# Optimization experiments

Measured on AMD Instinct MI355X. Metric: run time of the kernel, lower is better.

The kernel has to match this reference:

```python
import jax, jax.numpy as jnp
import numpy as np

B, N, F_IN = 2, 2048, 256
HEADS, F_OUT = 8, 32
NEG_SLOPE = 0.01  # torch F.leaky_relu default


def setup_inputs() -> dict:
    key = jax.random.key(0)
    k1, k2, k3, k4 = jax.random.split(key, 4)
    stdv = 1.0 / np.sqrt(F_OUT * HEADS)
    h = jax.random.normal(k1, (B, N, F_IN), dtype=jnp.float32)
    adj = jax.random.uniform(k2, (B, N, N), dtype=jnp.float32)
    W = jax.random.normal(k3, (F_IN, F_OUT * HEADS), dtype=jnp.float32) * stdv
    a = jax.random.normal(k4, (2 * F_OUT, 1), dtype=jnp.float32) * stdv
    return {"h": h, "adj": adj, "W": W, "a": a}


def reference(h, adj, W, a):
    # adj is accepted by the original forward but never used (dense attention).
    b, n, _ = h.shape
    f = a.shape[0] // 2
    heads = W.shape[1] // f
    Wh = (h @ W).reshape(b, n, heads, f)            # [b,n,h,f]
    a1 = a[:f, 0]                                    # attends to source i
    a2 = a[f:, 0]                                    # attends to target j
    e1 = jnp.einsum('bnhf,f->bhn', Wh, a1)           # [b,h,n]
    e2 = jnp.einsum('bnhf,f->bhn', Wh, a2)           # [b,h,n]
    # e[b,h,i,j] = leaky_relu(a1.Wh_i + a2.Wh_j) == a^T [Wh_i || Wh_j]
    e = jax.nn.leaky_relu(e1[:, :, :, None] + e2[:, :, None, :], NEG_SLOPE)
    att = jax.nn.softmax(e, axis=-1)                 # softmax over neighbors j
    h_prime = jnp.einsum('bhij,bjhf->bihf', att, Wh)  # [b,n,h,f]
    return h_prime.reshape(b, n, heads * f)
```

## Files before the change

kernel.cpp:

```cpp
#include <hip/hip_runtime.h>
#include <math.h>

#define BATCH 2
#define NTOK  2048
#define FIN   256
#define HEADS 8
#define FOUT  32
#define BH    (BATCH*HEADS)
#define NCOL  (HEADS*FOUT)
#define ROWS  (BATCH*NTOK)

typedef _Float16 f16;
typedef _Float16 f16x8 __attribute__((ext_vector_type(8)));
typedef float    f32x4 __attribute__((ext_vector_type(4)));

static const size_t OFF_E1   = 1048576;
static const size_t OFF_E2   = OFF_E1 + 32768;
static const size_t OFF_SKEY = OFF_E2 + 32768;
static const size_t OFF_SIDX = OFF_SKEY + 32768;
static const size_t OFF_W1S  = OFF_SIDX + 32768;
static const size_t OFF_W2S  = OFF_W1S + 32768;
static const size_t OFF_S1   = OFF_W2S + 32768;
static const size_t OFF_P2   = OFF_S1 + 32784;
static const size_t OFF_V1   = OFF_P2 + 32784;
static const size_t OFF_P2V  = OFF_V1 + 16u*2049u*32u;
static const size_t OFF_PART = OFF_V1;

__global__ __launch_bounds__(512) void k_mm(const float* __restrict__ h,
                                            const float* __restrict__ W,
                                            const float* __restrict__ av,
                                            float* __restrict__ Wh,
                                            float* __restrict__ e1, float* __restrict__ e2) {
    const int tid  = threadIdx.x;
    const int hh   = tid >> 6;
    const int lane = tid & 63;
    const int r    = lane & 15;
    const int q    = lane >> 4;
    const int row0 = blockIdx.x * 16;
    const int colA = hh * 32;

    const float* pa = h + (size_t)(row0 + r) * FIN + q * 8;
    const float HS = 16.0f, WS = 4096.0f;

    f32x4 acc[2];
    acc[0] = (f32x4){0.f,0.f,0.f,0.f};
    acc[1] = (f32x4){0.f,0.f,0.f,0.f};

    for (int ks = 0; ks < 8; ++ks) {
        const int kb = ks * 32;
        const float4 a0 = *(const float4*)(pa + kb);
        const float4 a1 = *(const float4*)(pa + kb + 4);
        const float ax[8] = {a0.x,a0.y,a0.z,a0.w,a1.x,a1.y,a1.z,a1.w};
        f16x8 ahi, alo;
        #pragma unroll
        for (int j = 0; j < 8; ++j) {
            float xv = ax[j] * HS;
            f16 hv = (f16)xv;
            ahi[j] = hv; alo[j] = (f16)(xv - (float)hv);
        }
        f16x8 bhi[2], blo[2];
        #pragma unroll
        for (int t = 0; t < 2; ++t) {
            const float* pb = W + (size_t)(kb + q * 8) * NCOL + colA + t * 16 + r;
            #pragma unroll
            for (int j = 0; j < 8; ++j) {
                float xv = pb[(size_t)j * NCOL] * WS;
                f16 hv = (f16)xv;
                bhi[t][j] = hv; blo[t][j] = (f16)(xv - (float)hv);
            }
        }
        #pragma unroll
        for (int t = 0; t < 2; ++t) {
            acc[t] = __builtin_amdgcn_mfma_f32_16x16x32_f16(ahi, bhi[t], acc[t], 0, 0, 0);
            acc[t] = __builtin_amdgcn_mfma_f32_16x16x32_f16(ahi, blo[t], acc[t], 0, 0, 0);
            acc[t] = __builtin_amdgcn_mfma_f32_16x16x32_f16(alo, bhi[t], acc[t], 0, 0, 0);
        }
    }

    const float SC = 1.0f / 65536.0f;
    acc[0] *= SC; acc[1] *= SC;

    #pragma unroll
    for (int t = 0; t < 2; ++t)
        #pragma unroll
        for (int g = 0; g < 4; ++g)
            Wh[(size_t)(row0 + q * 4 + g) * NCOL + colA + t * 16 + r] = acc[t][g];

    const float a10 = av[r], a11 = av[16 + r];
    const float a20 = av[32 + r], a21 = av[48 + r];
    float p1[4], p2[4];
    #pragma unroll
    for (int g = 0; g < 4; ++g) {
        p1[g] = acc[0][g] * a10 + acc[1][g] * a11;
        p2[g] = acc[0][g] * a20 + acc[1][g] * a21;
    }
    #pragma unroll
    for (int m = 1; m < 16; m <<= 1)
        #pragma unroll
        for (int g = 0; g < 4; ++g) {
            p1[g] += __shfl_xor(p1[g], m, 64);
            p2[g] += __shfl_xor(p2[g], m, 64);
        }
    if (r == 0) {
        #pragma unroll
        for (int g = 0; g < 4; ++g) {
            const int row = row0 + q * 4 + g;
            const int b   = row >> 11;
            const int n   = row & (NTOK - 1);
            e1[(b * HEADS + hh) * NTOK + n] = p1[g];
            e2[(b * HEADS + hh) * NTOK + n] = p2[g];
        }
    }
}

__device__ __forceinline__ unsigned long long sortkey(float f, int j) {
    unsigned int b = __float_as_uint(f);
    unsigned int u = (b & 0x80000000u) ? ~b : (b | 0x80000000u);
    return ((unsigned long long)u << 32) | (unsigned int)(NTOK - 1 - j);
}

__global__ __launch_bounds__(256) void k_rank8(const float* __restrict__ e2g,
                                               int* __restrict__ partial) {
    __shared__ alignas(16) unsigned long long ch[256];
    const int tid = threadIdx.x;
    const int bh  = blockIdx.x;
    const int kt  = blockIdx.y;
    const int jh  = blockIdx.z;
    const int kbase = kt * 256;
    ch[tid] = sortkey(e2g[bh * NTOK + kbase + tid], kbase + tid);
    __syncthreads();

    const int j0 = jh * 1024 + tid * 4;
    const float4 mv = *(const float4*)(e2g + bh * NTOK + j0);
    const unsigned long long my0 = sortkey(mv.x, j0);
    const unsigned long long my1 = sortkey(mv.y, j0 + 1);
    const unsigned long long my2 = sortkey(mv.z, j0 + 2);
    const unsigned long long my3 = sortkey(mv.w, j0 + 3);
    int r0 = 0, r1 = 0, r2 = 0, r3 = 0;
    const ulonglong2* c2 = (const ulonglong2*)ch;
    #pragma unroll 8
    for (int qq = 0; qq < 128; ++qq) {
        ulonglong2 v = c2[qq];
        r0 += (v.x > my0) + (v.y > my0);
        r1 += (v.x > my1) + (v.y > my1);
        r2 += (v.x > my2) + (v.y > my2);
        r3 += (v.x > my3) + (v.y > my3);
    }
    *(int4*)(partial + (size_t)(kt * BH + bh) * NTOK + j0) = make_int4(r0, r1, r2, r3);
}

__global__ __launch_bounds__(256) void k_scatter(const float* __restrict__ e2g,
                                                 const int* __restrict__ partial,
                                                 float* __restrict__ skey,
                                                 int* __restrict__ sidx,
                                                 float* __restrict__ w1s,
                                                 float* __restrict__ w2s) {
    const int tid = threadIdx.x;
    const int bh  = blockIdx.x;
    const int jt  = blockIdx.y;
    const int j   = jt * 256 + tid;
    int rank = 0;
    #pragma unroll
    for (int kt = 0; kt < 8; ++kt)
        rank += partial[(size_t)(kt * BH + bh) * NTOK + j];
    const float my = e2g[bh * NTOK + j];
    skey[bh * NTOK + rank] = my;
    sidx[bh * NTOK + rank] = j;
    w1s[bh * NTOK + rank]  = expf(my);
    w2s[bh * NTOK + rank]  = expf(0.01f * my);
}

__global__ __launch_bounds__(1024) void k_vscan(const float* __restrict__ Wh,
                                                const int* __restrict__ sidx,
                                                const float* __restrict__ w1s,
                                                const float* __restrict__ w2s,
                                                float* __restrict__ V1,
                                                float* __restrict__ P2V,
                                                float* __restrict__ S1,
                                                float* __restrict__ P2) {
    __shared__ float4 wtot[16];
    __shared__ float4 woff[16];
    const int t    = threadIdx.x;
    const int lane = t & 63;
    const int wv   = t >> 6;
    const int fg   = blockIdx.x;
    const int bh   = blockIdx.y;
    const int b    = bh >> 3;
    const int hh   = bh & 7;
    const int j0   = 2 * t;

    const float w1_0 = w1s[bh * NTOK + j0], w1_1 = w1s[bh * NTOK + j0 + 1];
    const float w2_0 = w2s[bh * NTOK + j0], w2_1 = w2s[bh * NTOK + j0 + 1];
    float4 g0, g1;
    if (fg < 8) {
        const int sj0 = sidx[bh * NTOK + j0];
        const int sj1 = sidx[bh * NTOK + j0 + 1];
        g0 = *(const float4*)(Wh + (size_t)(b * NTOK + sj0) * NCOL + hh * FOUT + fg * 4);
        g1 = *(const float4*)(Wh + (size_t)(b * NTOK + sj1) * NCOL + hh * FOUT + fg * 4);
    } else {
        g0 = make_float4(1.f, 0.f, 0.f, 0.f);
        g1 = make_float4(1.f, 0.f, 0.f, 0.f);
    }

    #pragma unroll 1
    for (int z = 0; z < 2; ++z) {
        const float w0  = z ? w2_0 : w1_0;
        const float w1v = z ? w2_1 : w1_1;
        float4 v0 = make_float4(w0 * g0.x,  w0 * g0.y,  w0 * g0.z,  w0 * g0.w);
        float4 v1 = make_float4(w1v * g1.x, w1v * g1.y, w1v * g1.z, w1v * g1.w);

        float4 s = make_float4(v0.x + v1.x, v0.y + v1.y, v0.z + v1.z, v0.w + v1.w);
        #pragma unroll
        for (int d = 1; d < 64; d <<= 1) {
            float ux = __shfl_up(s.x, (unsigned)d, 64);
            float uy = __shfl_up(s.y, (unsigned)d, 64);
            float uz = __shfl_up(s.z, (unsigned)d, 64);
            float uw = __shfl_up(s.w, (unsigned)d, 64);
            if (lane >= d) { s.x += ux; s.y += uy; s.z += uz; s.w += uw; }
        }
        float4 pair = make_float4(v0.x + v1.x, v0.y + v1.y, v0.z + v1.z, v0.w + v1.w);
        float4 excl = make_float4(s.x - pair.x, s.y - pair.y, s.z - pair.z, s.w - pair.w);
        if (lane == 63) wtot[wv] = s;
        __syncthreads();
        if (t < 16) {
            float4 ws = wtot[t];
            float4 inc = ws;
            #pragma unroll
            for (int d = 1; d < 16; d <<= 1) {
                float ux = __shfl_up(inc.x, (unsigned)d, 16);
                float uy = __shfl_up(inc.y, (unsigned)d, 16);
                float uz = __shfl_up(inc.z, (unsigned)d, 16);
                float uw = __shfl_up(inc.w, (unsigned)d, 16);
                if ((t & 15) >= d) { inc.x += ux; inc.y += uy; inc.z += uz; inc.w += uw; }
            }
            woff[t] = make_float4(inc.x - ws.x, inc.y - ws.y, inc.z - ws.z, inc.w - ws.w);
        }
        __syncthreads();

        float4 base = woff[wv];
        float4 i0 = make_float4(base.x + excl.x + v0.x, base.y + excl.y + v0.y,
                                base.z + excl.z + v0.z, base.w + excl.w + v0.w);
        float4 i1 = make_float4(i0.x + v1.x, i0.y + v1.y, i0.z + v1.z, i0.w + v1.w);

        if (fg < 8) {
            float* dst = z ? P2V : V1;
            float* plane = dst + ((size_t)bh * 8 + fg) * (2049u * 4u);
            *(float4*)(plane + (size_t)(j0 + 1) * 4) = i0;
            *(float4*)(plane + (size_t)(j0 + 2) * 4) = i1;
            if (t == 0)
                *(float4*)plane = make_float4(0.f, 0.f, 0.f, 0.f);
        } else {
            float* dst = z ? P2 : S1;
            dst[bh * 2049 + j0 + 1] = i0.x;
            dst[bh * 2049 + j0 + 2] = i1.x;
            if (t == 0) dst[bh * 2049] = 0.f;
        }
        __syncthreads();
    }
}

__global__ __launch_bounds__(256) void k_out(const float* __restrict__ skey,
                                             const float* __restrict__ e1g,
                                             const float* __restrict__ S1,
                                             const float* __restrict__ P2,
                                             const float* __restrict__ V1,
                                             const float* __restrict__ P2V,
                                             float* __restrict__ out) {
    __shared__ float keys[NTOK];
    const int tid = threadIdx.x;
    const int it  = blockIdx.x;
    const int bh  = blockIdx.y;
    const int b   = bh >> 3;
    const int hh  = bh & 7;
    #pragma unroll
    for (int q = 0; q < 8; ++q)
        keys[q * 256 + tid] = skey[bh * NTOK + q * 256 + tid];
    __syncthreads();

    const int i  = it * 32 + (tid >> 3);
    const int fg = tid & 7;
    const float e1v = e1g[bh * NTOK + i];
    const float th  = -e1v;
    int lo = 0, hi = NTOK;
    while (lo < hi) {
        int mid = (lo + hi) >> 1;
        if (keys[mid] > th) lo = mid + 1; else hi = mid;
    }
    const int k = lo;
    const float A = expf(e1v);
    const float C = expf(0.01f * e1v);
    const float s1  = S1[bh * 2049 + k];
    const float p2k = P2[bh * 2049 + k];
    const float p2t = P2[bh * 2049 + 2048];
    const float l   = A * s1 + C * (p2t - p2k);
    const float inv = 1.0f / l;
    const float* v1p  = V1  + ((size_t)bh * 8 + fg) * (2049u * 4u);
    const float* p2vp = P2V + ((size_t)bh * 8 + fg) * (2049u * 4u);
    float4 v1   = *(const float4*)(v1p  + (size_t)k * 4);
    float4 p2v  = *(const float4*)(p2vp + (size_t)k * 4);
    float4 p2vt = *(const float4*)(p2vp + (size_t)2048 * 4);
    float4 o;
    o.x = (A * v1.x + C * (p2vt.x - p2v.x)) * inv;
    o.y = (A * v1.y + C * (p2vt.y - p2v.y)) * inv;
    o.z = (A * v1.z + C * (p2vt.z - p2v.z)) * inv;
    o.w = (A * v1.w + C * (p2vt.w - p2v.w)) * inv;
    *(float4*)(out + (size_t)(b * NTOK + i) * NCOL + hh * FOUT + fg * 4) = o;
}

extern "C" void kernel_launch(void* const* d_in, const int* in_sizes, int n_in,
                              void* d_out, int out_size, void* d_ws, size_t ws_size,
                              hipStream_t stream) {
    const float* h = (const float*)d_in[0];
    const float* W = (const float*)d_in[2];
    const float* a = (const float*)d_in[3];
    float* out = (float*)d_out;
    float* ws  = (float*)d_ws;

    float* Wh   = ws;
    float* e1   = ws + OFF_E1;
    float* e2   = ws + OFF_E2;
    float* skey = ws + OFF_SKEY;
    int*   sidx = (int*)(ws + OFF_SIDX);
    float* w1s  = ws + OFF_W1S;
    float* w2s  = ws + OFF_W2S;
    float* S1   = ws + OFF_S1;
    float* P2   = ws + OFF_P2;
    float* V1   = ws + OFF_V1;
    float* P2V  = ws + OFF_P2V;
    int*   part = (int*)(ws + OFF_PART);

    k_mm     <<<256,               512, 0, stream>>>(h, W, a, Wh, e1, e2);
    k_rank8  <<<dim3(BH, 8, 2),    256, 0, stream>>>(e2, part);
    k_scatter<<<dim3(BH, 8),       256, 0, stream>>>(e2, part, skey, sidx, w1s, w2s);
    k_vscan  <<<dim3(9, BH),      1024, 0, stream>>>(Wh, sidx, w1s, w2s, V1, P2V, S1, P2);
    k_out    <<<dim3(NTOK/32, BH), 256, 0, stream>>>(skey, e1, S1, P2, V1, P2V, out);
}
```

Before: 116.6 us.

## Fuse five stage kernels into one cooperative kernel with grid syncs

Merges the matmul, rank, scatter, prefix-scan and output kernels into a single cooperative launch of 256 blocks of 512 threads, with grid.sync between stages. The goal is to remove the launch overhead and inter-kernel gaps of five small launches. The scan stage now gives each thread four elements with 512 threads per block, and the output stage handles four row tiles per block. The cost is idle threads in several stages (for example, only 256 of 512 threads work in rank/scatter) plus the grid-sync overhead, and the design relies on all 256 blocks being co-resident.

```diff
diff --git a/kernel.cpp b/kernel.cpp
--- a/kernel.cpp
+++ b/kernel.cpp
@@ -1,5 +1,8 @@
 #include <hip/hip_runtime.h>
+#include <hip/hip_cooperative_groups.h>
 #include <math.h>
+
+namespace cg = cooperative_groups;
 
 #define BATCH 2
 #define NTOK  2048
@@ -26,285 +29,303 @@
 static const size_t OFF_P2V  = OFF_V1 + 16u*2049u*32u;
 static const size_t OFF_PART = OFF_V1;
 
-__global__ __launch_bounds__(512) void k_mm(const float* __restrict__ h,
-                                            const float* __restrict__ W,
-                                            const float* __restrict__ av,
-                                            float* __restrict__ Wh,
-                                            float* __restrict__ e1, float* __restrict__ e2) {
-    const int tid  = threadIdx.x;
-    const int hh   = tid >> 6;
-    const int lane = tid & 63;
-    const int r    = lane & 15;
-    const int q    = lane >> 4;
-    const int row0 = blockIdx.x * 16;
-    const int colA = hh * 32;
-
-    const float* pa = h + (size_t)(row0 + r) * FIN + q * 8;
-    const float HS = 16.0f, WS = 4096.0f;
-
-    f32x4 acc[2];
-    acc[0] = (f32x4){0.f,0.f,0.f,0.f};
-    acc[1] = (f32x4){0.f,0.f,0.f,0.f};
-
-    for (int ks = 0; ks < 8; ++ks) {
-        const int kb = ks * 32;
-        const float4 a0 = *(const float4*)(pa + kb);
-        const float4 a1 = *(const float4*)(pa + kb + 4);
-        const float ax[8] = {a0.x,a0.y,a0.z,a0.w,a1.x,a1.y,a1.z,a1.w};
-        f16x8 ahi, alo;
-        #pragma unroll
-        for (int j = 0; j < 8; ++j) {
-            float xv = ax[j] * HS;
-            f16 hv = (f16)xv;
-            ahi[j] = hv; alo[j] = (f16)(xv - (float)hv);
-        }
-        f16x8 bhi[2], blo[2];
-        #pragma unroll
-        for (int t = 0; t < 2; ++t) {
-            const float* pb = W + (size_t)(kb + q * 8) * NCOL + colA + t * 16 + r;
-            #pragma unroll
-            for (int j = 0; j < 8; ++j) {
-                float xv = pb[(size_t)j * NCOL] * WS;
-                f16 hv = (f16)xv;
-                bhi[t][j] = hv; blo[t][j] = (f16)(xv - (float)hv);
-            }
-        }
-        #pragma unroll
-        for (int t = 0; t < 2; ++t) {
-            acc[t] = __builtin_amdgcn_mfma_f32_16x16x32_f16(ahi, bhi[t], acc[t], 0, 0, 0);
-            acc[t] = __builtin_amdgcn_mfma_f32_16x16x32_f16(ahi, blo[t], acc[t], 0, 0, 0);
-            acc[t] = __builtin_amdgcn_mfma_f32_16x16x32_f16(alo, bhi[t], acc[t], 0, 0, 0);
-        }
-    }
-
-    const float SC = 1.0f / 65536.0f;
-    acc[0] *= SC; acc[1] *= SC;
-
-    #pragma unroll
-    for (int t = 0; t < 2; ++t)
-        #pragma unroll
-        for (int g = 0; g < 4; ++g)
-            Wh[(size_t)(row0 + q * 4 + g) * NCOL + colA + t * 16 + r] = acc[t][g];
-
-    const float a10 = av[r], a11 = av[16 + r];
-    const float a20 = av[32 + r], a21 = av[48 + r];
-    float p1[4], p2[4];
-    #pragma unroll
-    for (int g = 0; g < 4; ++g) {
-        p1[g] = acc[0][g] * a10 + acc[1][g] * a11;
-        p2[g] = acc[0][g] * a20 + acc[1][g] * a21;
-    }
-    #pragma unroll
-    for (int m = 1; m < 16; m <<= 1)
-        #pragma unroll
-        for (int g = 0; g < 4; ++g) {
-            p1[g] += __shfl_xor(p1[g], m, 64);
-            p2[g] += __shfl_xor(p2[g], m, 64);
-        }
-    if (r == 0) {
-        #pragma unroll
-        for (int g = 0; g < 4; ++g) {
-            const int row = row0 + q * 4 + g;
-            const int b   = row >> 11;
-            const int n   = row & (NTOK - 1);
-            e1[(b * HEADS + hh) * NTOK + n] = p1[g];
-            e2[(b * HEADS + hh) * NTOK + n] = p2[g];
-        }
-    }
-}
-
 __device__ __forceinline__ unsigned long long sortkey(float f, int j) {
     unsigned int b = __float_as_uint(f);
     unsigned int u = (b & 0x80000000u) ? ~b : (b | 0x80000000u);
     return ((unsigned long long)u << 32) | (unsigned int)(NTOK - 1 - j);
 }
 
-__global__ __launch_bounds__(256) void k_rank8(const float* __restrict__ e2g,
-                                               int* __restrict__ partial) {
+__global__ __launch_bounds__(512) void k_mega(const float* __restrict__ h,
+                                              const float* __restrict__ W,
+                                              const float* __restrict__ av,
+                                              float* __restrict__ Wh,
+                                              float* __restrict__ e1, float* __restrict__ e2,
+                                              float* __restrict__ skey, int* __restrict__ sidx,
+                                              float* __restrict__ w1s, float* __restrict__ w2s,
+                                              float* __restrict__ S1, float* __restrict__ P2g,
+                                              float* __restrict__ V1, float* __restrict__ P2V,
+                                              int* __restrict__ partial,
+                                              float* __restrict__ out) {
+    cg::grid_group grid = cg::this_grid();
+    __shared__ float skeys[NTOK];
     __shared__ alignas(16) unsigned long long ch[256];
+    __shared__ float4 wtot[8];
+    __shared__ float4 woff[8];
+
     const int tid = threadIdx.x;
-    const int bh  = blockIdx.x;
-    const int kt  = blockIdx.y;
-    const int jh  = blockIdx.z;
-    const int kbase = kt * 256;
-    ch[tid] = sortkey(e2g[bh * NTOK + kbase + tid], kbase + tid);
-    __syncthreads();
-
-    const int j0 = jh * 1024 + tid * 4;
-    const float4 mv = *(const float4*)(e2g + bh * NTOK + j0);
-    const unsigned long long my0 = sortkey(mv.x, j0);
-    const unsigned long long my1 = sortkey(mv.y, j0 + 1);
-    const unsigned long long my2 = sortkey(mv.z, j0 + 2);
-    const unsigned long long my3 = sortkey(mv.w, j0 + 3);
-    int r0 = 0, r1 = 0, r2 = 0, r3 = 0;
-    const ulonglong2* c2 = (const ulonglong2*)ch;
-    #pragma unroll 8
-    for (int qq = 0; qq < 128; ++qq) {
-        ulonglong2 v = c2[qq];
-        r0 += (v.x > my0) + (v.y > my0);
-        r1 += (v.x > my1) + (v.y > my1);
-        r2 += (v.x > my2) + (v.y > my2);
-        r3 += (v.x > my3) + (v.y > my3);
-    }
-    *(int4*)(partial + (size_t)(kt * BH + bh) * NTOK + j0) = make_int4(r0, r1, r2, r3);
-}
-
-__global__ __launch_bounds__(256) void k_scatter(const float* __restrict__ e2g,
-                                                 const int* __restrict__ partial,
-                                                 float* __restrict__ skey,
-                                                 int* __restrict__ sidx,
-                                                 float* __restrict__ w1s,
-                                                 float* __restrict__ w2s) {
-    const int tid = threadIdx.x;
-    const int bh  = blockIdx.x;
-    const int jt  = blockIdx.y;
-    const int j   = jt * 256 + tid;
-    int rank = 0;
-    #pragma unroll
-    for (int kt = 0; kt < 8; ++kt)
-        rank += partial[(size_t)(kt * BH + bh) * NTOK + j];
-    const float my = e2g[bh * NTOK + j];
-    skey[bh * NTOK + rank] = my;
-    sidx[bh * NTOK + rank] = j;
-    w1s[bh * NTOK + rank]  = expf(my);
-    w2s[bh * NTOK + rank]  = expf(0.01f * my);
-}
-
-__global__ __launch_bounds__(1024) void k_vscan(const float* __restrict__ Wh,
-                                                const int* __restrict__ sidx,
-                                                const float* __restrict__ w1s,
-                                                const float* __restrict__ w2s,
-                                                float* __restrict__ V1,
-                                                float* __restrict__ P2V,
-                                                float* __restrict__ S1,
-                                                float* __restrict__ P2) {
-    __shared__ float4 wtot[16];
-    __shared__ float4 woff[16];
-    const int t    = threadIdx.x;
-    const int lane = t & 63;
-    const int wv   = t >> 6;
-    const int fg   = blockIdx.x;
-    const int bh   = blockIdx.y;
-    const int b    = bh >> 3;
-    const int hh   = bh & 7;
-    const int j0   = 2 * t;
-
-    const float w1_0 = w1s[bh * NTOK + j0], w1_1 = w1s[bh * NTOK + j0 + 1];
-    const float w2_0 = w2s[bh * NTOK + j0], w2_1 = w2s[bh * NTOK + j0 + 1];
-    float4 g0, g1;
-    if (fg < 8) {
-        const int sj0 = sidx[bh * NTOK + j0];
-        const int sj1 = sidx[bh * NTOK + j0 + 1];
-        g0 = *(const float4*)(Wh + (size_t)(b * NTOK + sj0) * NCOL + hh * FOUT + fg * 4);
-        g1 = *(const float4*)(Wh + (size_t)(b * NTOK + sj1) * NCOL + hh * FOUT + fg * 4);
-    } else {
-        g0 = make_float4(1.f, 0.f, 0.f, 0.f);
-        g1 = make_float4(1.f, 0.f, 0.f, 0.f);
-    }
-
-    #pragma unroll 1
-    for (int z = 0; z < 2; ++z) {
-        const float w0  = z ? w2_0 : w1_0;
-        const float w1v = z ? w2_1 : w1_1;
-        float4 v0 = make_float4(w0 * g0.x,  w0 * g0.y,  w0 * g0.z,  w0 * g0.w);
-        float4 v1 = make_float4(w1v * g1.x, w1v * g1.y, w1v * g1.z, w1v * g1.w);
-
-        float4 s = make_float4(v0.x + v1.x, v0.y + v1.y, v0.z + v1.z, v0.w + v1.w);
-        #pragma unroll
-        for (int d = 1; d < 64; d <<= 1) {
-            float ux = __shfl_up(s.x, (unsigned)d, 64);
-            float uy = __shfl_up(s.y, (unsigned)d, 64);
-            float uz = __shfl_up(s.z, (unsigned)d, 64);
-            float uw = __shfl_up(s.w, (unsigned)d, 64);
-            if (lane >= d) { s.x += ux; s.y += uy; s.z += uz; s.w += uw; }
-        }
-        float4 pair = make_float4(v0.x + v1.x, v0.y + v1.y, v0.z + v1.z, v0.w + v1.w);
-        float4 excl = make_float4(s.x - pair.x, s.y - pair.y, s.z - pair.z, s.w - pair.w);
-        if (lane == 63) wtot[wv] = s;
+    const int bid = blockIdx.x;
+
+    {
+        const int hh   = tid >> 6;
+        const int lane = tid & 63;
+        const int r    = lane & 15;
+        const int q    = lane >> 4;
+        const int row0 = bid * 16;
+        const int colA = hh * 32;
+
+        const float* pa = h + (size_t)(row0 + r) * FIN + q * 8;
+        const float HS = 16.0f, WS = 4096.0f;
+
+        f32x4 acc[2];
+        acc[0] = (f32x4){0.f,0.f,0.f,0.f};
+        acc[1] = (f32x4){0.f,0.f,0.f,0.f};
+
+        for (int ks = 0; ks < 8; ++ks) {
+            const int kb = ks * 32;
+            const float4 a0 = *(const float4*)(pa + kb);
+            const float4 a1 = *(const float4*)(pa + kb + 4);
+            const float ax[8] = {a0.x,a0.y,a0.z,a0.w,a1.x,a1.y,a1.z,a1.w};
+            f16x8 ahi, alo;
+            #pragma unroll
+            for (int j = 0; j < 8; ++j) {
+                float xv = ax[j] * HS;
+                f16 hv = (f16)xv;
+                ahi[j] = hv; alo[j] = (f16)(xv - (float)hv);
+            }
+            f16x8 bhi[2], blo[2];
+            #pragma unroll
+            for (int t = 0; t < 2; ++t) {
+                const float* pb = W + (size_t)(kb + q * 8) * NCOL + colA + t * 16 + r;
+                #pragma unroll
+                for (int j = 0; j < 8; ++j) {
+                    float xv = pb[(size_t)j * NCOL] * WS;
+                    f16 hv = (f16)xv;
+                    bhi[t][j] = hv; blo[t][j] = (f16)(xv - (float)hv);
+                }
+            }
+            #pragma unroll
+            for (int t = 0; t < 2; ++t) {
+                acc[t] = __builtin_amdgcn_mfma_f32_16x16x32_f16(ahi, bhi[t], acc[t], 0, 0, 0);
+                acc[t] = __builtin_amdgcn_mfma_f32_16x16x32_f16(ahi, blo[t], acc[t], 0, 0, 0);
+                acc[t] = __builtin_amdgcn_mfma_f32_16x16x32_f16(alo, bhi[t], acc[t], 0, 0, 0);
+            }
+        }
+
+        const float SC = 1.0f / 65536.0f;
+        acc[0] *= SC; acc[1] *= SC;
+
+        #pragma unroll
+        for (int t = 0; t < 2; ++t)
+            #pragma unroll
+            for (int g = 0; g < 4; ++g)
+                Wh[(size_t)(row0 + q * 4 + g) * NCOL + colA + t * 16 + r] = acc[t][g];
+
+        const float a10 = av[r], a11 = av[16 + r];
+        const float a20 = av[32 + r], a21 = av[48 + r];
+        float p1[4], p2[4];
+        #pragma unroll
+        for (int g = 0; g < 4; ++g) {
+            p1[g] = acc[0][g] * a10 + acc[1][g] * a11;
+            p2[g] = acc[0][g] * a20 + acc[1][g] * a21;
+        }
+        #pragma unroll
+        for (int m = 1; m < 16; m <<= 1)
+            #pragma unroll
+            for (int g = 0; g < 4; ++g) {
+                p1[g] += __shfl_xor(p1[g], m, 64);
+                p2[g] += __shfl_xor(p2[g], m, 64);
+            }
+        if (r == 0) {
+            #pragma unroll
+            for (int g = 0; g < 4; ++g) {
+                const int row = row0 + q * 4 + g;
+                const int b   = row >> 11;
+                const int n   = row & (NTOK - 1);
+                e1[(b * HEADS + hh) * NTOK + n] = p1[g];
+                e2[(b * HEADS + hh) * NTOK + n] = p2[g];
+            }
+        }
+    }
+    grid.sync();
+
+    {
+        const int bh = bid & 15;
+        const int kt = (bid >> 4) & 7;
+        const int jh = bid >> 7;
+        const int kbase = kt * 256;
+        if (tid < 256)
+            ch[tid] = sortkey(e2[bh * NTOK + kbase + tid], kbase + tid);
         __syncthreads();
-        if (t < 16) {
-            float4 ws = wtot[t];
-            float4 inc = ws;
-            #pragma unroll
-            for (int d = 1; d < 16; d <<= 1) {
-                float ux = __shfl_up(inc.x, (unsigned)d, 16);
-                float uy = __shfl_up(inc.y, (unsigned)d, 16);
-                float uz = __shfl_up(inc.z, (unsigned)d, 16);
-                float uw = __shfl_up(inc.w, (unsigned)d, 16);
-                if ((t & 15) >= d) { inc.x += ux; inc.y += uy; inc.z += uz; inc.w += uw; }
-            }
-            woff[t] = make_float4(inc.x - ws.x, inc.y - ws.y, inc.z - ws.z, inc.w - ws.w);
-        }
+        if (tid < 256) {
+            const int j0 = jh * 1024 + tid * 4;
+            const float4 mv = *(const float4*)(e2 + bh * NTOK + j0);
+            const unsigned long long my0 = sortkey(mv.x, j0);
+            const unsigned long long my1 = sortkey(mv.y, j0 + 1);
+            const unsigned long long my2 = sortkey(mv.z, j0 + 2);
+            const unsigned long long my3 = sortkey(mv.w, j0 + 3);
+            int r0 = 0, r1 = 0, r2 = 0, r3 = 0;
+            const ulonglong2* c2 = (const ulonglong2*)ch;
+            #pragma unroll 8
+            for (int qq = 0; qq < 128; ++qq) {
+                ulonglong2 v = c2[qq];
+                r0 += (v.x > my0) + (v.y > my0);
+                r1 += (v.x > my1) + (v.y > my1);
+                r2 += (v.x > my2) + (v.y > my2);
+                r3 += (v.x > my3) + (v.y > my3);
+            }
+            *(int4*)(partial + (size_t)(kt * BH + bh) * NTOK + j0) = make_int4(r0, r1, r2, r3);
+        }
+    }
+    grid.sync();
+
+    if (bid < 128 && tid < 256) {
+        const int bh = bid & 15;
+        const int jt = bid >> 4;
+        const int j  = jt * 256 + tid;
+        int rank = 0;
+        #pragma unroll
+        for (int kt = 0; kt < 8; ++kt)
+            rank += partial[(size_t)(kt * BH + bh) * NTOK + j];
+        const float my = e2[bh * NTOK + j];
+        skey[bh * NTOK + rank] = my;
+        sidx[bh * NTOK + rank] = j;
+        w1s[bh * NTOK + rank]  = expf(my);
+        w2s[bh * NTOK + rank]  = expf(0.01f * my);
+    }
+    grid.sync();
+
+    if (bid < 144) {
+        const int fg = bid >> 4;
+        const int bh = bid & 15;
+        const int b  = bh >> 3;
+        const int hh = bh & 7;
+        const int lane = tid & 63;
+        const int wv   = tid >> 6;
+        const int j0   = 4 * tid;
+
+        float w1v[4], w2v[4];
+        float4 g[4];
+        #pragma unroll
+        for (int i = 0; i < 4; ++i) {
+            w1v[i] = w1s[bh * NTOK + j0 + i];
+            w2v[i] = w2s[bh * NTOK + j0 + i];
+        }
+        if (fg < 8) {
+            #pragma unroll
+            for (int i = 0; i < 4; ++i) {
+                const int sj = sidx[bh * NTOK + j0 + i];
+                g[i] = *(const float4*)(Wh + (size_t)(b * NTOK + sj) * NCOL + hh * FOUT + fg * 4);
+            }
+        } else {
+            #pragma unroll
+            for (int i = 0; i < 4; ++i) g[i] = make_float4(1.f, 0.f, 0.f, 0.f);
+        }
+
+        #pragma unroll 1
+        for (int z = 0; z < 2; ++z) {
+            float4 v[4];
+            #pragma unroll
+            for (int i = 0; i < 4; ++i) {
+                const float w = z ? w2v[i] : w1v[i];
+                v[i] = make_float4(w * g[i].x, w * g[i].y, w * g[i].z, w * g[i].w);
+            }
+            float4 s = make_float4(v[0].x + v[1].x + v[2].x + v[3].x,
+                                   v[0].y + v[1].y + v[2].y + v[3].y,
+                                   v[0].z + v[1].z + v[2].z + v[3].z,
+                                   v[0].w + v[1].w + v[2].w + v[3].w);
+            const float4 quad = s;
+            #pragma unroll
+            for (int d = 1; d < 64; d <<= 1) {
+                float ux = __shfl_up(s.x, (unsigned)d, 64);
+                float uy = __shfl_up(s.y, (unsigned)d, 64);
+                float uz = __shfl_up(s.z, (unsigned)d, 64);
+                float uw = __shfl_up(s.w, (unsigned)d, 64);
+                if (lane >= d) { s.x += ux; s.y += uy; s.z += uz; s.w += uw; }
+            }
+            float4 excl = make_float4(s.x - quad.x, s.y - quad.y, s.z - quad.z, s.w - quad.w);
+            if (lane == 63) wtot[wv] = s;
+            __syncthreads();
+            if (tid < 8) {
+                float4 ws = wtot[tid];
+                float4 inc = ws;
+                #pragma unroll
+                for (int d = 1; d < 8; d <<= 1) {
+                    float ux = __shfl_up(inc.x, (unsigned)d, 8);
+                    float uy = __shfl_up(inc.y, (unsigned)d, 8);
+                    float uz = __shfl_up(inc.z, (unsigned)d, 8);
+                    float uw = __shfl_up(inc.w, (unsigned)d, 8);
+                    if ((tid & 7) >= d) { inc.x += ux; inc.y += uy; inc.z += uz; inc.w += uw; }
+                }
+                woff[tid] = make_float4(inc.x - ws.x, inc.y - ws.y, inc.z - ws.z, inc.w - ws.w);
+            }
+            __syncthreads();
+
+            float4 base = woff[wv];
+            float4 run = make_float4(base.x + excl.x, base.y + excl.y,
+                                     base.z + excl.z, base.w + excl.w);
+            float4 io[4];
+            #pragma unroll
+            for (int i = 0; i < 4; ++i) {
+                run = make_float4(run.x + v[i].x, run.y + v[i].y,
+                                  run.z + v[i].z, run.w + v[i].w);
+                io[i] = run;
+            }
+
+            if (fg < 8) {
+                float* dst = z ? P2V : V1;
+                float* plane = dst + ((size_t)bh * 8 + fg) * (2049u * 4u);
+                #pragma unroll
+                for (int i = 0; i < 4; ++i)
+                    *(float4*)(plane + (size_t)(j0 + 1 + i) * 4) = io[i];
+                if (tid == 0)
+                    *(float4*)plane = make_float4(0.f, 0.f, 0.f, 0.f);
+            } else {
+                float* dst = z ? P2g : S1;
+                #pragma unroll
+                for (int i = 0; i < 4; ++i)
+                    dst[bh * 2049 + j0 + 1 + i] = io[i].x;
+                if (tid == 0) dst[bh * 2049] = 0.f;
+            }
+            __syncthreads();
+        }
+    }
+    grid.sync();
+
+    {
+        const int bh     = bid & 15;
+        const int itbase = (bid >> 4) * 4;
+        const int b      = bh >> 3;
+        const int hh     = bh & 7;
+        #pragma unroll
+        for (int q = 0; q < 4; ++q)
+            skeys[q * 512 + tid] = skey[bh * NTOK + q * 512 + tid];
         __syncthreads();
 
-        float4 base = woff[wv];
-        float4 i0 = make_float4(base.x + excl.x + v0.x, base.y + excl.y + v0.y,
-                                base.z + excl.z + v0.z, base.w + excl.w + v0.w);
-        float4 i1 = make_float4(i0.x + v1.x, i0.y + v1.y, i0.z + v1.z, i0.w + v1.w);
-
-        if (fg < 8) {
-            float* dst = z ? P2V : V1;
-            float* plane = dst + ((size_t)bh * 8 + fg) * (2049u * 4u);
-            *(float4*)(plane + (size_t)(j0 + 1) * 4) = i0;
-            *(float4*)(plane + (size_t)(j0 + 2) * 4) = i1;
-            if (t == 0)
-                *(float4*)plane = make_float4(0.f, 0.f, 0.f, 0.f);
-        } else {
-            float* dst = z ? P2 : S1;
-            dst[bh * 2049 + j0 + 1] = i0.x;
-            dst[bh * 2049 + j0 + 2] = i1.x;
-            if (t == 0) dst[bh * 2049] = 0.f;
-        }
-        __syncthreads();
-    }
-}
-
-__global__ __launch_bounds__(256) void k_out(const float* __restrict__ skey,
-                                             const float* __restrict__ e1g,
-                                             const float* __restrict__ S1,
-                                             const float* __restrict__ P2,
-                                             const float* __restrict__ V1,
-                                             const float* __restrict__ P2V,
-                                             float* __restrict__ out) {
-    __shared__ float keys[NTOK];
-    const int tid = threadIdx.x;
-    const int it  = blockIdx.x;
-    const int bh  = blockIdx.y;
-    const int b   = bh >> 3;
-    const int hh  = bh & 7;
-    #pragma unroll
-    for (int q = 0; q < 8; ++q)
-        keys[q * 256 + tid] = skey[bh * NTOK + q * 256 + tid];
-    __syncthreads();
-
-    const int i  = it * 32 + (tid >> 3);
-    const int fg = tid & 7;
-    const float e1v = e1g[bh * NTOK + i];
-    const float th  = -e1v;
-    int lo = 0, hi = NTOK;
-    while (lo < hi) {
-        int mid = (lo + hi) >> 1;
-        if (keys[mid] > th) lo = mid + 1; else hi = mid;
-    }
-    const int k = lo;
-    const float A = expf(e1v);
-    const float C = expf(0.01f * e1v);
-    const float s1  = S1[bh * 2049 + k];
-    const float p2k = P2[bh * 2049 + k];
-    const float p2t = P2[bh * 2049 + 2048];
-    const float l   = A * s1 + C * (p2t - p2k);
-    const float inv = 1.0f / l;
-    const float* v1p  = V1  + ((size_t)bh * 8 + fg) * (2049u * 4u);
-    const float* p2vp = P2V + ((size_t)bh * 8 + fg) * (2049u * 4u);
-    float4 v1   = *(const float4*)(v1p  + (size_t)k * 4);
-    float4 p2v  = *(const float4*)(p2vp + (size_t)k * 4);
-    float4 p2vt = *(const float4*)(p2vp + (size_t)2048 * 4);
-    float4 o;
-    o.x = (A * v1.x + C * (p2vt.x - p2v.x)) * inv;
-    o.y = (A * v1.y + C * (p2vt.y - p2v.y)) * inv;
-    o.z = (A * v1.z + C * (p2vt.z - p2v.z)) * inv;
-    o.w = (A * v1.w + C * (p2vt.w - p2v.w)) * inv;
-    *(float4*)(out + (size_t)(b * NTOK + i) * NCOL + hh * FOUT + fg * 4) = o;
+        const int unit = tid >> 8;
+        const int ut   = tid & 255;
+        #pragma unroll
+        for (int s = 0; s < 2; ++s) {
+            const int it = itbase + s * 2 + unit;
+            const int i  = it * 32 + (ut >> 3);
+            const int fg = ut & 7;
+            const float e1v = e1[bh * NTOK + i];
+            const float th  = -e1v;
+            int lo = 0, hi = NTOK;
+            while (lo < hi) {
+                int mid = (lo + hi) >> 1;
+                if (skeys[mid] > th) lo = mid + 1; else hi = mid;
+            }
+            const int k = lo;
+            const float A = expf(e1v);
+            const float C = expf(0.01f * e1v);
+            const float s1  = S1[bh * 2049 + k];
+            const float p2k = P2g[bh * 2049 + k];
+            const float p2t = P2g[bh * 2049 + 2048];
+            const float l   = A * s1 + C * (p2t - p2k);
+            const float inv = 1.0f / l;
+            const float* v1p  = V1  + ((size_t)bh * 8 + fg) * (2049u * 4u);
+            const float* p2vp = P2V + ((size_t)bh * 8 + fg) * (2049u * 4u);
+            float4 v1   = *(const float4*)(v1p  + (size_t)k * 4);
+            float4 p2v  = *(const float4*)(p2vp + (size_t)k * 4);
+            float4 p2vt = *(const float4*)(p2vp + (size_t)2048 * 4);
+            float4 o;
+            o.x = (A * v1.x + C * (p2vt.x - p2v.x)) * inv;
+            o.y = (A * v1.y + C * (p2vt.y - p2v.y)) * inv;
+            o.z = (A * v1.z + C * (p2vt.z - p2v.z)) * inv;
+            o.w = (A * v1.w + C * (p2vt.w - p2v.w)) * inv;
+            *(float4*)(out + (size_t)(b * NTOK + i) * NCOL + hh * FOUT + fg * 4) = o;
+        }
+    }
 }
 
 extern "C" void kernel_launch(void* const* d_in, const int* in_sizes, int n_in,
@@ -329,9 +350,10 @@
     float* P2V  = ws + OFF_P2V;
     int*   part = (int*)(ws + OFF_PART);
 
-    k_mm     <<<256,               512, 0, stream>>>(h, W, a, Wh, e1, e2);
-    k_rank8  <<<dim3(BH, 8, 2),    256, 0, stream>>>(e2, part);
-    k_scatter<<<dim3(BH, 8),       256, 0, stream>>>(e2, part, skey, sidx, w1s, w2s);
-    k_vscan  <<<dim3(9, BH),      1024, 0, stream>>>(Wh, sidx, w1s, w2s, V1, P2V, S1, P2);
-    k_out    <<<dim3(NTOK/32, BH), 256, 0, stream>>>(skey, e1, S1, P2, V1, P2V, out);
+    void* args[] = { (void*)&h, (void*)&W, (void*)&a, (void*)&Wh, (void*)&e1, (void*)&e2,
+                     (void*)&skey, (void*)&sidx, (void*)&w1s, (void*)&w2s,
+                     (void*)&S1, (void*)&P2, (void*)&V1, (void*)&P2V,
+                     (void*)&part, (void*)&out };
+    hipLaunchCooperativeKernel((const void*)k_mega, dim3(256), dim3(512),
+                               args, 0, stream);
 }
```

Result: slower. 237.2 us (+103.4%).
